# Kernel tuning notes

Measured on AMD Instinct MI355X. Metric: run time of the kernel, lower is better.

The kernel has to match this reference:

```python
import jax, jax.numpy as jnp
import numpy as np

N = 50000      # nodes
E = 800000     # edges
F_IN = 128     # input features
H = 64         # hidden channels
G = 64         # graphs in batch
EPS = 1e-5


def setup_inputs() -> dict:
    key = jax.random.key(0)
    ks = jax.random.split(key, 24)
    def nrm(k, s):
        return jax.random.normal(k, s, dtype=jnp.float32) * 0.05
    inp = {
        "x": nrm(ks[0], (N, F_IN)),
        "edge_index": jax.random.randint(ks[1], (2, E), 0, N),
        "batch": jnp.sort(jax.random.randint(ks[2], (N,), 0, G)),
        # GCNConv weights (stored [in, out]; math equivalent to torch Linear)
        "W0": nrm(ks[3], (F_IN, H)), "b0": nrm(ks[4], (H,)),
        "W1": nrm(ks[5], (H, H)),    "b1": nrm(ks[6], (H,)),
        "W2": nrm(ks[7], (H, H)),    "b2": nrm(ks[8], (H,)),
        # residual linears
        "RW0": nrm(ks[9], (F_IN, H)),  "rb0": nrm(ks[10], (H,)),
        "RW1": nrm(ks[11], (H, H)),    "rb1": nrm(ks[12], (H,)),
        "RW2": nrm(ks[13], (H, H)),    "rb2": nrm(ks[14], (H,)),
        # layernorm gamma/beta
        "g0": jnp.ones((H,), jnp.float32), "be0": jnp.zeros((H,), jnp.float32),
        "g1": jnp.ones((H,), jnp.float32), "be1": jnp.zeros((H,), jnp.float32),
        "g2": jnp.ones((H,), jnp.float32), "be2": jnp.zeros((H,), jnp.float32),
        # final readout linear
        "lw": nrm(ks[15], (H, 1)), "lb": nrm(ks[16], (1,)),
    }
    return inp


def _layernorm(x, g, b):
    mu = jnp.mean(x, axis=-1, keepdims=True)
    var = jnp.mean(jnp.square(x - mu), axis=-1, keepdims=True)
    return (x - mu) * jax.lax.rsqrt(var + EPS) * g + b


def reference(x, edge_index, batch,
              W0, b0, W1, b1, W2, b2,
              RW0, rb0, RW1, rb1, RW2, rb2,
              g0, be0, g1, be1, g2, be2,
              lw, lb):
    n = x.shape[0]
    loops = jnp.arange(n)
    row = jnp.concatenate([edge_index[0], loops])  # source
    col = jnp.concatenate([edge_index[1], loops])  # target
    # symmetric GCN normalization with self-loops (PyG gcn_norm)
    deg = jax.ops.segment_sum(jnp.ones_like(col, dtype=x.dtype), col, num_segments=n)
    dis = jnp.where(deg > 0, deg ** -0.5, 0.0)
    norm = dis[row] * dis[col]  # [E+N]

    params = [(W0, b0, RW0, rb0, g0, be0),
              (W1, b1, RW1, rb1, g1, be1),
              (W2, b2, RW2, rb2, g2, be2)]
    n_layers = len(params)
    for i, (W, b, RW, rb, g, be) in enumerate(params):
        h = x @ W                                                  # [n, H]
        agg = jax.ops.segment_sum(h[row] * norm[:, None], col, num_segments=n) + b
        x = agg + (x @ RW + rb)                                    # residual
        # dropout: eval mode -> identity
        x = _layernorm(x, g, be)
        if i < n_layers - 1:
            x = jax.nn.relu(x)

    # global mean pool over graphs
    counts = jax.ops.segment_sum(jnp.ones((n,), x.dtype), batch, num_segments=G)
    pooled = jax.ops.segment_sum(x, batch, num_segments=G) / jnp.maximum(counts, 1.0)[:, None]
    return pooled @ lw + lb  # [G, 1]
```

## Files before the change

kernel.cpp:

```cpp
#include <hip/hip_runtime.h>
#include <hip/hip_bf16.h>

#define HID 64
#define NGRAPH 64
#define BSH 7
#define NCH 384

static inline size_t align256(size_t x) { return (x + 255) & ~(size_t)255; }

typedef __attribute__((ext_vector_type(8))) short bf16x8;
typedef __attribute__((ext_vector_type(4))) float f32x4;

__device__ __forceinline__ float ldf(const void* p, size_t i, int f32) {
    if (f32) return ((const float*)p)[i];
    unsigned int w = ((unsigned int)((const unsigned short*)p)[i]) << 16;
    return __uint_as_float(w);
}
__device__ __forceinline__ float bf2f(unsigned short u) {
    return __uint_as_float(((unsigned int)u) << 16);
}
__device__ __forceinline__ unsigned short f2bf(float f) {
    __hip_bfloat16 h = __float2bfloat16(f);
    return *(unsigned short*)&h;
}

__device__ __forceinline__ unsigned char f2e4m3(float f) {
#if defined(__has_builtin) && __has_builtin(__builtin_amdgcn_cvt_pk_fp8_f32)
    int r = __builtin_amdgcn_cvt_pk_fp8_f32(f, f, 0, false);
    return (unsigned char)(r & 0xFF);
#else
    unsigned u = __float_as_uint(f);
    unsigned s = (u >> 24) & 0x80;
    unsigned a = u & 0x7FFFFFFF;
    float af = __uint_as_float(a);
    if (af < 0.015625f) {
        int m = (int)rintf(af * 512.f);
        return (unsigned char)(s | m);
    }
    unsigned r = a + 0x7FFFF + ((a >> 20) & 1);
    int e = (int)(r >> 23) - 127;
    if (e > 8) return (unsigned char)(s | 0x7E);
    return (unsigned char)(s | ((e + 7) << 3) | ((r >> 20) & 7));
#endif
}
template <int IDX>
__device__ __forceinline__ float d8(unsigned p) {
#if defined(__has_builtin) && __has_builtin(__builtin_amdgcn_cvt_f32_fp8)
    return __builtin_amdgcn_cvt_f32_fp8(p, IDX);
#else
    unsigned b = (p >> (IDX * 8)) & 0xFF;
    unsigned e = (b >> 3) & 0xF, m = b & 7;
    float v = e ? __uint_as_float(((e + 120) << 23) | (m << 20))
                : (float)m * (1.f / 512.f);
    return (b & 0x80) ? -v : v;
#endif
}

__global__ void k_sniff(const unsigned short* __restrict__ x, int nwords, int* __restrict__ flag,
                        float* __restrict__ gsum, int* __restrict__ gcnt) {
    __shared__ int cw, cz;
    int t = threadIdx.x;
    if (t == 0) { cw = 0; cz = 0; }
    if (t < NGRAPH) { gsum[t] = 0.f; gcnt[t] = 0; }
    __syncthreads();
    int weird = 0, evenzero = 0;
    for (int i = t; i < nwords; i += blockDim.x) {
        unsigned short u = x[i];
        int e = (u >> 7) & 0xFF;
        if (e >= 128) weird++;
        if (((i & 1) == 0) && ((u & 0x7FFF) == 0)) evenzero++;
    }
    atomicAdd(&cw, weird);
    atomicAdd(&cz, evenzero);
    __syncthreads();
    if (t == 0) *flag = (cw > nwords / 16 || cz > nwords / 8) ? 1 : 0;
}

__global__ __launch_bounds__(256) void k_prep(const int* __restrict__ batch, int* __restrict__ gcnt,
                                              int n, int nbG,
                                              const void* W0, const void* RW0, const void* b0, const void* rb0,
                                              const void* W1, const void* RW1, const void* b1, const void* rb1,
                                              const void* W2, const void* RW2, const void* b2, const void* rb2,
                                              const int* __restrict__ dflag,
                                              unsigned short* wt0, unsigned short* wt1, unsigned short* wt2,
                                              float* bcat,
                                              const int* __restrict__ ecol, int e, int nbuck,
                                              int* __restrict__ hist) {
    __shared__ int sh[1024];
    int b = blockIdx.x, t = threadIdx.x;
    if (b < nbG) {
        if (t < NGRAPH) sh[t] = 0;
        __syncthreads();
        int i = b * 256 + t;
        if (i < n) atomicAdd(&sh[batch[i]], 1);
        __syncthreads();
        if (t < NGRAPH && sh[t] > 0) atomicAdd(&gcnt[t], sh[t]);
    } else if (b < nbG + 130) {
        int f = *dflag;
        int i = (b - nbG) * 256 + t;
        if (i < 16384) {
            int nn = i >> 7, k = i & 127;
            float v = (nn < 64) ? ldf(W0, (size_t)k * 64 + nn, f) : ldf(RW0, (size_t)k * 64 + (nn - 64), f);
            wt0[nn * 128 + k] = f2bf(v);
        } else if (i < 24576) {
            int j = i - 16384; int nn = j >> 6, k = j & 63;
            float v = (nn < 64) ? ldf(W1, (size_t)k * 64 + nn, f) : ldf(RW1, (size_t)k * 64 + (nn - 64), f);
            wt1[nn * 64 + k] = f2bf(v);
        } else if (i < 32768) {
            int j = i - 24576; int nn = j >> 6, k = j & 63;
            float v = (nn < 64) ? ldf(W2, (size_t)k * 64 + nn, f) : ldf(RW2, (size_t)k * 64 + (nn - 64), f);
            wt2[nn * 64 + k] = f2bf(v);
        } else if (i < 32768 + 192) {
            int j = i - 32768; int l = j >> 6, c = j & 63;
            const void* bb = (l == 0) ? b0 : (l == 1) ? b1 : b2;
            const void* rr = (l == 0) ? rb0 : (l == 1) ? rb1 : rb2;
            bcat[l * 64 + c] = ldf(bb, c, f) + ldf(rr, c, f);
        }
    } else {
        int c = b - nbG - 130;
        for (int i = t; i < nbuck; i += 256) sh[i] = 0;
        __syncthreads();
        int per = (e + NCH - 1) / NCH;
        int s = c * per, en = min(e, s + per);
        for (int i = s + t; i < en; i += 256)
            atomicAdd(&sh[ecol[i] >> BSH], 1);
        __syncthreads();
        for (int i = t; i < nbuck; i += 256) hist[i * NCH + c] = sh[i];
    }
}

__global__ void k_scan1(const int* __restrict__ src, int* __restrict__ bsum, int n) {
    __shared__ int s[256];
    int t = threadIdx.x;
    int base = blockIdx.x * 1024 + t * 4;
    int sum = 0;
#pragma unroll
    for (int j = 0; j < 4; j++) { int i = base + j; if (i < n) sum += src[i]; }
    s[t] = sum;
    __syncthreads();
    for (int o = 128; o > 0; o >>= 1) {
        if (t < o) s[t] += s[t + o];
        __syncthreads();
    }
    if (t == 0) bsum[blockIdx.x] = s[0];
}

__global__ void k_scan2(const int* __restrict__ bsum, int* __restrict__ bscan,
                        int* __restrict__ out, int nb, int n) {
    __shared__ int s[256];
    int t = threadIdx.x;
    int v = (t < nb) ? bsum[t] : 0;
    s[t] = v;
    __syncthreads();
    for (int o = 1; o < 256; o <<= 1) {
        int x = (t >= o) ? s[t - o] : 0;
        __syncthreads();
        s[t] += x;
        __syncthreads();
    }
    if (t < nb) bscan[t] = s[t] - v;
    if (t == nb - 1) out[n] = s[t];
}

__global__ void k_scan3(const int* __restrict__ src, const int* __restrict__ bscan,
                        int* __restrict__ out, int n) {
    __shared__ int s[256];
    int t = threadIdx.x;
    int base = blockIdx.x * 1024 + t * 4;
    int tsum = 0;
#pragma unroll
    for (int j = 0; j < 4; j++) { int i = base + j; if (i < n) tsum += src[i]; }
    s[t] = tsum;
    __syncthreads();
    for (int o = 1; o < 256; o <<= 1) {
        int x = (t >= o) ? s[t - o] : 0;
        __syncthreads();
        s[t] += x;
        __syncthreads();
    }
    int off = bscan[blockIdx.x] + s[t] - tsum;
#pragma unroll
    for (int j = 0; j < 4; j++) {
        int i = base + j;
        if (i < n) { out[i] = off; off += src[i]; }
    }
}

__global__ __launch_bounds__(512) void k_scatter(const int* __restrict__ erow,
                                                 const int* __restrict__ ecol, int e, int nbuck,
                                                 const int* __restrict__ hoffs,
                                                 int* __restrict__ esrc,
                                                 unsigned char* __restrict__ et7) {
    __shared__ int cur[1024];
    int c = blockIdx.x, t = threadIdx.x;
    for (int i = t; i < nbuck; i += 512) cur[i] = hoffs[i * NCH + c];
    __syncthreads();
    int per = (e + NCH - 1) / NCH;
    int s = c * per, en = min(e, s + per);
    for (int i = s + t; i < en; i += 512) {
        int tg = ecol[i];
        int p = atomicAdd(&cur[tg >> BSH], 1);
        esrc[p] = erow[i];
        et7[p] = (unsigned char)(tg & 127);
    }
}

__global__ __launch_bounds__(256) void k_bucket(const int* __restrict__ esrc,
                                                const unsigned char* __restrict__ et7,
                                                const int* __restrict__ hoffs,
                                                int nbuck, int n, int e,
                                                int* __restrict__ offs, float* __restrict__ dis,
                                                int* __restrict__ csr) {
    __shared__ int hist[128];
    __shared__ int lofs[128];
    __shared__ int curs[128];
    int b = blockIdx.x, t = threadIdx.x;
    int nb0 = b << BSH;
    int nn = n - nb0; if (nn > 128) nn = 128;
    int s = hoffs[b * NCH];
    int en = (b + 1 < nbuck) ? hoffs[(b + 1) * NCH] : e;
    if (t < 128) hist[t] = 0;
    __syncthreads();
    for (int i = s + t; i < en; i += 256)
        atomicAdd(&hist[et7[i]], 1);
    __syncthreads();
    if (t < 128) lofs[t] = hist[t];
    __syncthreads();
    for (int o = 1; o < 128; o <<= 1) {
        int v = (t < 128 && t >= o) ? lofs[t - o] : 0;
        __syncthreads();
        if (t < 128) lofs[t] += v;
        __syncthreads();
    }
    if (t < nn) {
        int ex = s + lofs[t] - hist[t];
        offs[nb0 + t] = ex;
        curs[t] = ex;
        dis[nb0 + t] = rsqrtf((float)(hist[t] + 1));
    }
    if (b == nbuck - 1 && t == 0) offs[n] = e;
    __syncthreads();
    for (int i = s + t; i < en; i += 256) {
        int p = atomicAdd(&curs[et7[i]], 1);
        csr[p] = esrc[i];
    }
}

template <int K, bool XFLAG, bool LO>
__global__ __launch_bounds__(256) void k_gemm(const void* __restrict__ xin,
                                              const unsigned short* __restrict__ wt,
                                              const float* __restrict__ bcat,
                                              const float* __restrict__ dis,
                                              const int* __restrict__ dflag,
                                              unsigned char* __restrict__ hs,
                                              float* __restrict__ base, int n) {
    const int KP = K + 8;
    __shared__ unsigned short sXh[64 * KP];
    __shared__ unsigned short sXl[LO ? 64 * KP : 1];
    int f32 = *dflag;
    int tid = threadIdx.x;
    int row0 = blockIdx.x * 64;

    if (XFLAG && !f32) {
        const uint4* xv = (const uint4*)xin;
        const int C = K / 8;
        for (int i = tid; i < 64 * C; i += 256) {
            int r = i / C, c = i % C;
            int gr = row0 + r;
            uint4 v = (gr < n) ? xv[(size_t)gr * C + c] : make_uint4(0, 0, 0, 0);
            *(uint4*)&sXh[r * KP + c * 8] = v;
        }
    } else if (XFLAG) {
        for (int i = tid; i < 64 * K; i += 256) {
            int r = i / K, k = i - r * K;
            int gr = row0 + r;
            float v = (gr < n) ? ((const float*)xin)[(size_t)gr * K + k] : 0.f;
            sXh[r * KP + k] = f2bf(v);
        }
    } else {
        const float4* xv = (const float4*)xin;
        const int C = K / 4;
        for (int i = tid; i < 64 * C; i += 256) {
            int r = i / C, c = i % C;
            int gr = row0 + r;
            float4 v = (gr < n) ? xv[(size_t)gr * C + c] : make_float4(0.f, 0.f, 0.f, 0.f);
            ushort4 h, lo;
            h.x = f2bf(v.x); h.y = f2bf(v.y); h.z = f2bf(v.z); h.w = f2bf(v.w);
            if (LO) {
                lo.x = f2bf(v.x - bf2f(h.x)); lo.y = f2bf(v.y - bf2f(h.y));
                lo.z = f2bf(v.z - bf2f(h.z)); lo.w = f2bf(v.w - bf2f(h.w));
            }
            *(ushort4*)&sXh[r * KP + c * 4] = h;
            if (LO) *(ushort4*)&sXl[r * KP + c * 4] = lo;
        }
    }
    __syncthreads();

    int w = tid >> 6, lane = tid & 63;
    int m = lane & 15, q = lane >> 4;
    f32x4 acc[8];
#pragma unroll
    for (int ct = 0; ct < 8; ct++) acc[ct] = (f32x4){0.f, 0.f, 0.f, 0.f};

    int arow = w * 16 + m;
#pragma unroll
    for (int ks = 0; ks < K / 32; ks++) {
        int ka = ks * 32 + q * 8;
        bf16x8 ah = *(const bf16x8*)&sXh[arow * KP + ka];
        bf16x8 al;
        if (LO) al = *(const bf16x8*)&sXl[arow * KP + ka];
#pragma unroll
        for (int ct = 0; ct < 8; ct++) {
            bf16x8 bb = *(const bf16x8*)(wt + (size_t)(ct * 16 + m) * K + ka);
            acc[ct] = __builtin_amdgcn_mfma_f32_16x16x32_bf16(ah, bb, acc[ct], 0, 0, 0);
            if (LO) acc[ct] = __builtin_amdgcn_mfma_f32_16x16x32_bf16(al, bb, acc[ct], 0, 0, 0);
        }
    }

#pragma unroll
    for (int ct = 0; ct < 4; ct++) {
        int col = ct * 16 + m;
#pragma unroll
        for (int reg = 0; reg < 4; reg++) {
            int r = row0 + w * 16 + q * 4 + reg;
            if (r < n) {
                float dv = dis[r];
                float h = acc[ct][reg] * dv;
                hs[(size_t)r * 64 + col] = f2e4m3(h);
                base[(size_t)r * 64 + col] = h * dv + acc[ct + 4][reg] + bcat[col];
            }
        }
    }
}

template <bool FINAL>
__global__ __launch_bounds__(1024) void k_agg_ln(const unsigned char* __restrict__ hs,
                                                 const float* __restrict__ base,
                                                 const float* __restrict__ dis,
                                                 const int* __restrict__ offs,
                                                 const int* __restrict__ csr,
                                                 const void* __restrict__ gam,
                                                 const void* __restrict__ bet,
                                                 const int* __restrict__ dflag,
                                                 float* __restrict__ xout, int n, int relu,
                                                 const int* __restrict__ batch,
                                                 const void* __restrict__ lw,
                                                 float* __restrict__ gsum) {
    __shared__ float sG[FINAL ? NGRAPH : 1];
    int f32 = *dflag;
    int t = threadIdx.x;
    if (FINAL) {
        if (t < NGRAPH) sG[t] = 0.f;
        __syncthreads();
    }
    int grp = t >> 4;
    int l = t & 15;
    int gl0 = (t & 63) & ~15;
    int v = blockIdx.x * 64 + grp;
    if (v < n) {
        int s = offs[v];
        int e2 = offs[v + 1];
        float4 bv = *(const float4*)&base[(size_t)v * 64 + l * 4];
        float dv = dis[v];
        float a0 = 0.f, a1 = 0.f, a2 = 0.f, a3 = 0.f;
        for (int gbase = s; gbase < e2; gbase += 16) {
            int cnt = e2 - gbase; if (cnt > 16) cnt = 16;
            int cur = (gbase + l < e2) ? csr[gbase + l] : 0;
            if (cnt == 16) {
                unsigned pp[16];
#pragma unroll
                for (int j = 0; j < 16; j++) {
                    int sj = __shfl(cur, gl0 + j, 64);
                    pp[j] = *(const unsigned*)(hs + (size_t)sj * 64 + l * 4);
                }
#pragma unroll
                for (int j = 0; j < 16; j++) {
                    a0 += d8<0>(pp[j]);
                    a1 += d8<1>(pp[j]);
                    a2 += d8<2>(pp[j]);
                    a3 += d8<3>(pp[j]);
                }
            } else {
                int j = 0;
                for (; j + 7 < cnt; j += 8) {
                    unsigned pp[8];
#pragma unroll
                    for (int u = 0; u < 8; u++) {
                        int sj = __shfl(cur, gl0 + j + u, 64);
                        pp[u] = *(const unsigned*)(hs + (size_t)sj * 64 + l * 4);
                    }
#pragma unroll
                    for (int u = 0; u < 8; u++) {
                        a0 += d8<0>(pp[u]);
                        a1 += d8<1>(pp[u]);
                        a2 += d8<2>(pp[u]);
                        a3 += d8<3>(pp[u]);
                    }
                }
                for (; j + 3 < cnt; j += 4) {
                    unsigned pp[4];
#pragma unroll
                    for (int u = 0; u < 4; u++) {
                        int sj = __shfl(cur, gl0 + j + u, 64);
                        pp[u] = *(const unsigned*)(hs + (size_t)sj * 64 + l * 4);
                    }
#pragma unroll
                    for (int u = 0; u < 4; u++) {
                        a0 += d8<0>(pp[u]);
                        a1 += d8<1>(pp[u]);
                        a2 += d8<2>(pp[u]);
                        a3 += d8<3>(pp[u]);
                    }
                }
                for (; j < cnt; j++) {
                    int sj = __shfl(cur, gl0 + j, 64);
                    unsigned p0 = *(const unsigned*)(hs + (size_t)sj * 64 + l * 4);
                    a0 += d8<0>(p0);
                    a1 += d8<1>(p0);
                    a2 += d8<2>(p0);
                    a3 += d8<3>(p0);
                }
            }
        }
        a0 = bv.x + dv * a0;
        a1 = bv.y + dv * a1;
        a2 = bv.z + dv * a2;
        a3 = bv.w + dv * a3;
        float m = a0 + a1 + a2 + a3;
        m += __shfl_xor(m, 1, 64); m += __shfl_xor(m, 2, 64);
        m += __shfl_xor(m, 4, 64); m += __shfl_xor(m, 8, 64);
        m *= (1.f / 64.f);
        float d0 = a0 - m, d1 = a1 - m, d2 = a2 - m, d3 = a3 - m;
        float var = d0 * d0 + d1 * d1 + d2 * d2 + d3 * d3;
        var += __shfl_xor(var, 1, 64); var += __shfl_xor(var, 2, 64);
        var += __shfl_xor(var, 4, 64); var += __shfl_xor(var, 8, 64);
        var *= (1.f / 64.f);
        float rs = rsqrtf(var + 1e-5f);
        float y0 = d0 * rs * ldf(gam, l * 4 + 0, f32) + ldf(bet, l * 4 + 0, f32);
        float y1 = d1 * rs * ldf(gam, l * 4 + 1, f32) + ldf(bet, l * 4 + 1, f32);
        float y2 = d2 * rs * ldf(gam, l * 4 + 2, f32) + ldf(bet, l * 4 + 2, f32);
        float y3 = d3 * rs * ldf(gam, l * 4 + 3, f32) + ldf(bet, l * 4 + 3, f32);
        if (relu) {
            y0 = fmaxf(y0, 0.f); y1 = fmaxf(y1, 0.f);
            y2 = fmaxf(y2, 0.f); y3 = fmaxf(y3, 0.f);
        }
        if (!FINAL) {
            *(float4*)&xout[(size_t)v * 64 + l * 4] = make_float4(y0, y1, y2, y3);
        } else {
            float val = y0 * ldf(lw, l * 4 + 0, f32) + y1 * ldf(lw, l * 4 + 1, f32)
                      + y2 * ldf(lw, l * 4 + 2, f32) + y3 * ldf(lw, l * 4 + 3, f32);
            val += __shfl_xor(val, 1, 64); val += __shfl_xor(val, 2, 64);
            val += __shfl_xor(val, 4, 64); val += __shfl_xor(val, 8, 64);
            if (l == 0) atomicAdd(&sG[batch[v]], val);
        }
    }
    if (FINAL) {
        __syncthreads();
        if (t < NGRAPH && sG[t] != 0.f) atomicAdd(&gsum[t], sG[t]);
    }
}

__global__ void k_final(const float* __restrict__ gsum, const int* __restrict__ gcnt,
                        const void* __restrict__ lb, const int* __restrict__ dflag,
                        void* __restrict__ out, int g) {
    int f32 = *dflag;
    int i = threadIdx.x;
    if (i < g) {
        float c = fmaxf((float)gcnt[i], 1.f);
        float v = gsum[i] / c + ldf(lb, 0, f32);
        if (f32) ((float*)out)[i] = v;
        else ((__hip_bfloat16*)out)[i] = __float2bfloat16(v);
    }
}

extern "C" void kernel_launch(void* const* d_in, const int* in_sizes, int n_in,
                              void* d_out, int out_size, void* d_ws, size_t ws_size,
                              hipStream_t stream) {
    const void* x_in = d_in[0];
    const int* edge_index = (const int*)d_in[1];
    const int* batch = (const int*)d_in[2];
    const void *W0 = d_in[3], *b0 = d_in[4], *W1 = d_in[5], *b1 = d_in[6],
               *W2 = d_in[7], *b2 = d_in[8];
    const void *RW0 = d_in[9], *rb0 = d_in[10], *RW1 = d_in[11], *rb1 = d_in[12],
               *RW2 = d_in[13], *rb2 = d_in[14];
    const void *g0 = d_in[15], *be0 = d_in[16], *g1 = d_in[17], *be1 = d_in[18],
               *g2 = d_in[19], *be2 = d_in[20], *lw = d_in[21], *lb = d_in[22];

    const int N = in_sizes[2];
    const int E = in_sizes[1] / 2;
    const int* erow = edge_index;
    const int* ecol = edge_index + E;
    const int nbuck = (N + 127) >> BSH;
    const int T = nbuck * NCH;

    char* p = (char*)d_ws;
    size_t off = 0;
    float* dis = (float*)(p + off);  off = align256(off + (size_t)N * 4);
    int* offs = (int*)(p + off);     off = align256(off + (size_t)(N + 1) * 4);
    int* csr = (int*)(p + off);      off = align256(off + (size_t)E * 4);
    int* esrc = (int*)(p + off);     off = align256(off + (size_t)E * 4);
    unsigned char* et7 = (unsigned char*)(p + off); off = align256(off + (size_t)E);
    int* hist = (int*)(p + off);     off = align256(off + (size_t)T * 4);
    int* hoffs = (int*)(p + off);    off = align256(off + (size_t)(T + 1) * 4);
    unsigned char* hs = (unsigned char*)(p + off); off = align256(off + (size_t)N * HID);
    float* base = (float*)(p + off); off = align256(off + (size_t)N * HID * 4);
    float* xbuf = (float*)(p + off); off = align256(off + (size_t)N * HID * 4);
    unsigned short* wt0 = (unsigned short*)(p + off); off = align256(off + 16384 * 2);
    unsigned short* wt1 = (unsigned short*)(p + off); off = align256(off + 8192 * 2);
    unsigned short* wt2 = (unsigned short*)(p + off); off = align256(off + 8192 * 2);
    float* bcat = (float*)(p + off); off = align256(off + 192 * 4);
    int* bsum = (int*)(p + off);     off = align256(off + 256 * 4);
    int* bscan = (int*)(p + off);    off = align256(off + 256 * 4);
    float* gsum = (float*)(p + off); off = align256(off + NGRAPH * 4);
    int* gcnt = (int*)(p + off);     off = align256(off + NGRAPH * 4);
    int* dflag = (int*)(p + off);    off = align256(off + 4);
    (void)ws_size;

    const int TB = 256;
    int nbG = (N + TB - 1) / TB;
    int nbT = (T + 1023) / 1024;
    int nb_gemm = (N + 63) / 64;
    int nb_agg = (N + 63) / 64;

    k_sniff<<<1, 256, 0, stream>>>((const unsigned short*)x_in, 8192, dflag, gsum, gcnt);
    k_prep<<<nbG + 130 + NCH, TB, 0, stream>>>(batch, gcnt, N, nbG,
                                               W0, RW0, b0, rb0, W1, RW1, b1, rb1,
                                               W2, RW2, b2, rb2, dflag, wt0, wt1, wt2, bcat,
                                               ecol, E, nbuck, hist);
    k_scan1<<<nbT, TB, 0, stream>>>(hist, bsum, T);
    k_scan2<<<1, TB, 0, stream>>>(bsum, bscan, hoffs, nbT, T);
    k_scan3<<<nbT, TB, 0, stream>>>(hist, bscan, hoffs, T);
    k_scatter<<<NCH, 512, 0, stream>>>(erow, ecol, E, nbuck, hoffs, esrc, et7);
    k_bucket<<<nbuck, TB, 0, stream>>>(esrc, et7, hoffs, nbuck, N, E, offs, dis, csr);

    k_gemm<128, true, false><<<nb_gemm, TB, 0, stream>>>(x_in, wt0, bcat, dis, dflag, hs, base, N);
    k_agg_ln<false><<<nb_agg, 1024, 0, stream>>>(hs, base, dis, offs, csr, g0, be0, dflag,
                                                 xbuf, N, 1, nullptr, nullptr, nullptr);
    k_gemm<64, false, true><<<nb_gemm, TB, 0, stream>>>(xbuf, wt1, bcat + 64, dis, dflag, hs, base, N);
    k_agg_ln<false><<<nb_agg, 1024, 0, stream>>>(hs, base, dis, offs, csr, g1, be1, dflag,
                                                 xbuf, N, 1, nullptr, nullptr, nullptr);
    k_gemm<64, false, true><<<nb_gemm, TB, 0, stream>>>(xbuf, wt2, bcat + 128, dis, dflag, hs, base, N);
    k_agg_ln<true><<<nb_agg, 1024, 0, stream>>>(hs, base, dis, offs, csr, g2, be2, dflag,
                                                nullptr, N, 0, batch, lw, gsum);

    k_final<<<1, 64, 0, stream>>>(gsum, gcnt, lb, dflag, d_out, NGRAPH);
}
```

Before: 305.8 us.

## Fuse next-layer GEMM into aggregation-layernorm kernel and stage weights in LDS

The aggregation plus layernorm kernel now also runs the next layer's GEMM on its 64-row tile. It splits the normalized output into bf16 hi/lo parts in shared memory and runs MFMA against weights staged in LDS. This drops the fp32 xbuf round trip through global memory and two GEMM launches, using ping-pong hs/base buffers instead. The standalone layer-0 GEMM also stages its weights in LDS, and the scatter kernel drops from 512 to 256 threads per block. The costs are more LDS use and a barrier in the 1024-thread kernel, which may lower occupancy.

```diff
diff --git a/kernel.cpp b/kernel.cpp
--- a/kernel.cpp
+++ b/kernel.cpp
@@ -186,18 +186,18 @@
     }
 }
 
-__global__ __launch_bounds__(512) void k_scatter(const int* __restrict__ erow,
+__global__ __launch_bounds__(256) void k_scatter(const int* __restrict__ erow,
                                                  const int* __restrict__ ecol, int e, int nbuck,
                                                  const int* __restrict__ hoffs,
                                                  int* __restrict__ esrc,
                                                  unsigned char* __restrict__ et7) {
     __shared__ int cur[1024];
     int c = blockIdx.x, t = threadIdx.x;
-    for (int i = t; i < nbuck; i += 512) cur[i] = hoffs[i * NCH + c];
+    for (int i = t; i < nbuck; i += 256) cur[i] = hoffs[i * NCH + c];
     __syncthreads();
     int per = (e + NCH - 1) / NCH;
     int s = c * per, en = min(e, s + per);
-    for (int i = s + t; i < en; i += 512) {
+    for (int i = s + t; i < en; i += 256) {
         int tg = ecol[i];
         int p = atomicAdd(&cur[tg >> BSH], 1);
         esrc[p] = erow[i];
@@ -257,10 +257,21 @@
     const int KP = K + 8;
     __shared__ unsigned short sXh[64 * KP];
     __shared__ unsigned short sXl[LO ? 64 * KP : 1];
+    __shared__ unsigned short sW[128 * KP];
     int f32 = *dflag;
     int tid = threadIdx.x;
     int row0 = blockIdx.x * 64;
 
+    {
+        const uint4* src = (const uint4*)wt;
+        uint4* dst = (uint4*)sW;
+        const int C = K / 8;
+        const int CP = KP / 8;
+        for (int i = tid; i < 128 * C; i += 256) {
+            int nrow = i / C, c = i % C;
+            dst[nrow * CP + c] = src[i];
+        }
+    }
     if (XFLAG && !f32) {
         const uint4* xv = (const uint4*)xin;
         const int C = K / 8;
@@ -311,7 +322,7 @@
         if (LO) al = *(const bf16x8*)&sXl[arow * KP + ka];
 #pragma unroll
         for (int ct = 0; ct < 8; ct++) {
-            bf16x8 bb = *(const bf16x8*)(wt + (size_t)(ct * 16 + m) * K + ka);
+            bf16x8 bb = *(const bf16x8*)&sW[(ct * 16 + m) * KP + ka];
             acc[ct] = __builtin_amdgcn_mfma_f32_16x16x32_bf16(ah, bb, acc[ct], 0, 0, 0);
             if (LO) acc[ct] = __builtin_amdgcn_mfma_f32_16x16x32_bf16(al, bb, acc[ct], 0, 0, 0);
         }
@@ -333,93 +344,92 @@
     }
 }
 
-template <bool FINAL>
-__global__ __launch_bounds__(1024) void k_agg_ln(const unsigned char* __restrict__ hs,
-                                                 const float* __restrict__ base,
-                                                 const float* __restrict__ dis,
-                                                 const int* __restrict__ offs,
-                                                 const int* __restrict__ csr,
-                                                 const void* __restrict__ gam,
-                                                 const void* __restrict__ bet,
-                                                 const int* __restrict__ dflag,
-                                                 float* __restrict__ xout, int n, int relu,
-                                                 const int* __restrict__ batch,
-                                                 const void* __restrict__ lw,
-                                                 float* __restrict__ gsum) {
-    __shared__ float sG[FINAL ? NGRAPH : 1];
+template <bool GN>
+__global__ __launch_bounds__(1024) void k_fagg(const unsigned char* __restrict__ hs_in,
+                                               const float* __restrict__ base_in,
+                                               const float* __restrict__ dis,
+                                               const int* __restrict__ offs,
+                                               const int* __restrict__ csr,
+                                               const void* __restrict__ gam,
+                                               const void* __restrict__ bet,
+                                               const int* __restrict__ dflag,
+                                               int n, int relu,
+                                               const unsigned short* __restrict__ wt,
+                                               const float* __restrict__ bcat,
+                                               unsigned char* __restrict__ hs_out,
+                                               float* __restrict__ base_out,
+                                               const int* __restrict__ batch,
+                                               const void* __restrict__ lw,
+                                               float* __restrict__ gsum) {
+    __shared__ unsigned short sYh[GN ? 64 * 72 : 1];
+    __shared__ unsigned short sYl[GN ? 64 * 72 : 1];
+    __shared__ unsigned short sW[GN ? 128 * 72 : 1];
+    __shared__ float sG[GN ? 1 : NGRAPH];
+    int t = threadIdx.x;
     int f32 = *dflag;
-    int t = threadIdx.x;
-    if (FINAL) {
+    if (GN) {
+        const uint4* src = (const uint4*)wt;
+        uint4* dst = (uint4*)sW;
+        int nrow = t >> 3, c = t & 7;
+        dst[nrow * 9 + c] = src[t];
+    } else {
         if (t < NGRAPH) sG[t] = 0.f;
         __syncthreads();
     }
+
     int grp = t >> 4;
     int l = t & 15;
     int gl0 = (t & 63) & ~15;
-    int v = blockIdx.x * 64 + grp;
+    int row0 = blockIdx.x * 64;
+    int v = row0 + grp;
+    float y0 = 0.f, y1 = 0.f, y2 = 0.f, y3 = 0.f;
     if (v < n) {
         int s = offs[v];
         int e2 = offs[v + 1];
-        float4 bv = *(const float4*)&base[(size_t)v * 64 + l * 4];
+        float4 bv = *(const float4*)&base_in[(size_t)v * 64 + l * 4];
         float dv = dis[v];
         float a0 = 0.f, a1 = 0.f, a2 = 0.f, a3 = 0.f;
         for (int gbase = s; gbase < e2; gbase += 16) {
             int cnt = e2 - gbase; if (cnt > 16) cnt = 16;
             int cur = (gbase + l < e2) ? csr[gbase + l] : 0;
-            if (cnt == 16) {
-                unsigned pp[16];
-#pragma unroll
-                for (int j = 0; j < 16; j++) {
-                    int sj = __shfl(cur, gl0 + j, 64);
-                    pp[j] = *(const unsigned*)(hs + (size_t)sj * 64 + l * 4);
+            int j = 0;
+            for (; j + 7 < cnt; j += 8) {
+                unsigned pp[8];
+#pragma unroll
+                for (int u = 0; u < 8; u++) {
+                    int sj = __shfl(cur, gl0 + j + u, 64);
+                    pp[u] = *(const unsigned*)(hs_in + (size_t)sj * 64 + l * 4);
                 }
 #pragma unroll
-                for (int j = 0; j < 16; j++) {
-                    a0 += d8<0>(pp[j]);
-                    a1 += d8<1>(pp[j]);
-                    a2 += d8<2>(pp[j]);
-                    a3 += d8<3>(pp[j]);
+                for (int u = 0; u < 8; u++) {
+                    a0 += d8<0>(pp[u]);
+                    a1 += d8<1>(pp[u]);
+                    a2 += d8<2>(pp[u]);
+                    a3 += d8<3>(pp[u]);
                 }
-            } else {
-                int j = 0;
-                for (; j + 7 < cnt; j += 8) {
-                    unsigned pp[8];
-#pragma unroll
-                    for (int u = 0; u < 8; u++) {
-                        int sj = __shfl(cur, gl0 + j + u, 64);
-                        pp[u] = *(const unsigned*)(hs + (size_t)sj * 64 + l * 4);
-                    }
-#pragma unroll
-                    for (int u = 0; u < 8; u++) {
-                        a0 += d8<0>(pp[u]);
-                        a1 += d8<1>(pp[u]);
-                        a2 += d8<2>(pp[u]);
-                        a3 += d8<3>(pp[u]);
-                    }
+            }
+            for (; j + 3 < cnt; j += 4) {
+                unsigned pp[4];
+#pragma unroll
+                for (int u = 0; u < 4; u++) {
+                    int sj = __shfl(cur, gl0 + j + u, 64);
+                    pp[u] = *(const unsigned*)(hs_in + (size_t)sj * 64 + l * 4);
                 }
-                for (; j + 3 < cnt; j += 4) {
-                    unsigned pp[4];
-#pragma unroll
-                    for (int u = 0; u < 4; u++) {
-                        int sj = __shfl(cur, gl0 + j + u, 64);
-                        pp[u] = *(const unsigned*)(hs + (size_t)sj * 64 + l * 4);
-                    }
-#pragma unroll
-                    for (int u = 0; u < 4; u++) {
-                        a0 += d8<0>(pp[u]);
-                        a1 += d8<1>(pp[u]);
-                        a2 += d8<2>(pp[u]);
-                        a3 += d8<3>(pp[u]);
-                    }
+#pragma unroll
+                for (int u = 0; u < 4; u++) {
+                    a0 += d8<0>(pp[u]);
+                    a1 += d8<1>(pp[u]);
+                    a2 += d8<2>(pp[u]);
+                    a3 += d8<3>(pp[u]);
                 }
-                for (; j < cnt; j++) {
-                    int sj = __shfl(cur, gl0 + j, 64);
-                    unsigned p0 = *(const unsigned*)(hs + (size_t)sj * 64 + l * 4);
-                    a0 += d8<0>(p0);
-                    a1 += d8<1>(p0);
-                    a2 += d8<2>(p0);
-                    a3 += d8<3>(p0);
-                }
+            }
+            for (; j < cnt; j++) {
+                int sj = __shfl(cur, gl0 + j, 64);
+                unsigned p0 = *(const unsigned*)(hs_in + (size_t)sj * 64 + l * 4);
+                a0 += d8<0>(p0);
+                a1 += d8<1>(p0);
+                a2 += d8<2>(p0);
+                a3 += d8<3>(p0);
             }
         }
         a0 = bv.x + dv * a0;
@@ -436,27 +446,68 @@
         var += __shfl_xor(var, 4, 64); var += __shfl_xor(var, 8, 64);
         var *= (1.f / 64.f);
         float rs = rsqrtf(var + 1e-5f);
-        float y0 = d0 * rs * ldf(gam, l * 4 + 0, f32) + ldf(bet, l * 4 + 0, f32);
-        float y1 = d1 * rs * ldf(gam, l * 4 + 1, f32) + ldf(bet, l * 4 + 1, f32);
-        float y2 = d2 * rs * ldf(gam, l * 4 + 2, f32) + ldf(bet, l * 4 + 2, f32);
-        float y3 = d3 * rs * ldf(gam, l * 4 + 3, f32) + ldf(bet, l * 4 + 3, f32);
+        y0 = d0 * rs * ldf(gam, l * 4 + 0, f32) + ldf(bet, l * 4 + 0, f32);
+        y1 = d1 * rs * ldf(gam, l * 4 + 1, f32) + ldf(bet, l * 4 + 1, f32);
+        y2 = d2 * rs * ldf(gam, l * 4 + 2, f32) + ldf(bet, l * 4 + 2, f32);
+        y3 = d3 * rs * ldf(gam, l * 4 + 3, f32) + ldf(bet, l * 4 + 3, f32);
         if (relu) {
             y0 = fmaxf(y0, 0.f); y1 = fmaxf(y1, 0.f);
             y2 = fmaxf(y2, 0.f); y3 = fmaxf(y3, 0.f);
         }
-        if (!FINAL) {
-            *(float4*)&xout[(size_t)v * 64 + l * 4] = make_float4(y0, y1, y2, y3);
-        } else {
+    }
+
+    if (!GN) {
+        if (v < n) {
             float val = y0 * ldf(lw, l * 4 + 0, f32) + y1 * ldf(lw, l * 4 + 1, f32)
                       + y2 * ldf(lw, l * 4 + 2, f32) + y3 * ldf(lw, l * 4 + 3, f32);
             val += __shfl_xor(val, 1, 64); val += __shfl_xor(val, 2, 64);
             val += __shfl_xor(val, 4, 64); val += __shfl_xor(val, 8, 64);
             if (l == 0) atomicAdd(&sG[batch[v]], val);
         }
-    }
-    if (FINAL) {
         __syncthreads();
         if (t < NGRAPH && sG[t] != 0.f) atomicAdd(&gsum[t], sG[t]);
+        return;
+    }
+
+    {
+        ushort4 h, lo;
+        h.x = f2bf(y0); h.y = f2bf(y1); h.z = f2bf(y2); h.w = f2bf(y3);
+        lo.x = f2bf(y0 - bf2f(h.x)); lo.y = f2bf(y1 - bf2f(h.y));
+        lo.z = f2bf(y2 - bf2f(h.z)); lo.w = f2bf(y3 - bf2f(h.w));
+        if (v >= n) { h = make_ushort4(0, 0, 0, 0); lo = make_ushort4(0, 0, 0, 0); }
+        *(ushort4*)&sYh[grp * 72 + l * 4] = h;
+        *(ushort4*)&sYl[grp * 72 + l * 4] = lo;
+    }
+    __syncthreads();
+
+    int ww = t >> 6, lane = t & 63;
+    int m = lane & 15, q = lane >> 4;
+    int rt = ww & 3, c2 = ww >> 2;
+    f32x4 accW = (f32x4){0.f, 0.f, 0.f, 0.f};
+    f32x4 accR = (f32x4){0.f, 0.f, 0.f, 0.f};
+    int arow = rt * 16 + m;
+#pragma unroll
+    for (int ks = 0; ks < 2; ks++) {
+        int ka = ks * 32 + q * 8;
+        bf16x8 ah = *(const bf16x8*)&sYh[arow * 72 + ka];
+        bf16x8 al = *(const bf16x8*)&sYl[arow * 72 + ka];
+        bf16x8 bW = *(const bf16x8*)&sW[(c2 * 16 + m) * 72 + ka];
+        bf16x8 bR = *(const bf16x8*)&sW[((c2 + 4) * 16 + m) * 72 + ka];
+        accW = __builtin_amdgcn_mfma_f32_16x16x32_bf16(ah, bW, accW, 0, 0, 0);
+        accW = __builtin_amdgcn_mfma_f32_16x16x32_bf16(al, bW, accW, 0, 0, 0);
+        accR = __builtin_amdgcn_mfma_f32_16x16x32_bf16(ah, bR, accR, 0, 0, 0);
+        accR = __builtin_amdgcn_mfma_f32_16x16x32_bf16(al, bR, accR, 0, 0, 0);
+    }
+    int col = c2 * 16 + m;
+#pragma unroll
+    for (int reg = 0; reg < 4; reg++) {
+        int r = row0 + rt * 16 + q * 4 + reg;
+        if (r < n) {
+            float dv = dis[r];
+            float h = accW[reg] * dv;
+            hs_out[(size_t)r * 64 + col] = f2e4m3(h);
+            base_out[(size_t)r * 64 + col] = h * dv + accR[reg] + bcat[col];
+        }
     }
 }
 
@@ -502,9 +553,10 @@
     unsigned char* et7 = (unsigned char*)(p + off); off = align256(off + (size_t)E);
     int* hist = (int*)(p + off);     off = align256(off + (size_t)T * 4);
     int* hoffs = (int*)(p + off);    off = align256(off + (size_t)(T + 1) * 4);
-    unsigned char* hs = (unsigned char*)(p + off); off = align256(off + (size_t)N * HID);
-    float* base = (float*)(p + off); off = align256(off + (size_t)N * HID * 4);
-    float* xbuf = (float*)(p + off); off = align256(off + (size_t)N * HID * 4);
+    unsigned char* hsA = (unsigned char*)(p + off); off = align256(off + (size_t)N * HID);
+    unsigned char* hsB = (unsigned char*)(p + off); off = align256(off + (size_t)N * HID);
+    float* baseA = (float*)(p + off); off = align256(off + (size_t)N * HID * 4);
+    float* baseB = (float*)(p + off); off = align256(off + (size_t)N * HID * 4);
     unsigned short* wt0 = (unsigned short*)(p + off); off = align256(off + 16384 * 2);
     unsigned short* wt1 = (unsigned short*)(p + off); off = align256(off + 8192 * 2);
     unsigned short* wt2 = (unsigned short*)(p + off); off = align256(off + 8192 * 2);
@@ -530,18 +582,16 @@
     k_scan1<<<nbT, TB, 0, stream>>>(hist, bsum, T);
     k_scan2<<<1, TB, 0, stream>>>(bsum, bscan, hoffs, nbT, T);
     k_scan3<<<nbT, TB, 0, stream>>>(hist, bscan, hoffs, T);
-    k_scatter<<<NCH, 512, 0, stream>>>(erow, ecol, E, nbuck, hoffs, esrc, et7);
+    k_scatter<<<NCH, TB, 0, stream>>>(erow, ecol, E, nbuck, hoffs, esrc, et7);
     k_bucket<<<nbuck, TB, 0, stream>>>(esrc, et7, hoffs, nbuck, N, E, offs, dis, csr);
 
-    k_gemm<128, true, false><<<nb_gemm, TB, 0, stream>>>(x_in, wt0, bcat, dis, dflag, hs, base, N);
-    k_agg_ln<false><<<nb_agg, 1024, 0, stream>>>(hs, base, dis, offs, csr, g0, be0, dflag,
-                                                 xbuf, N, 1, nullptr, nullptr, nullptr);
-    k_gemm<64, false, true><<<nb_gemm, TB, 0, stream>>>(xbuf, wt1, bcat + 64, dis, dflag, hs, base, N);
-    k_agg_ln<false><<<nb_agg, 1024, 0, stream>>>(hs, base, dis, offs, csr, g1, be1, dflag,
-                                                 xbuf, N, 1, nullptr, nullptr, nullptr);
-    k_gemm<64, false, true><<<nb_gemm, TB, 0, stream>>>(xbuf, wt2, bcat + 128, dis, dflag, hs, base, N);
-    k_agg_ln<true><<<nb_agg, 1024, 0, stream>>>(hs, base, dis, offs, csr, g2, be2, dflag,
-                                                nullptr, N, 0, batch, lw, gsum);
+    k_gemm<128, true, false><<<nb_gemm, TB, 0, stream>>>(x_in, wt0, bcat, dis, dflag, hsA, baseA, N);
+    k_fagg<true><<<nb_agg, 1024, 0, stream>>>(hsA, baseA, dis, offs, csr, g0, be0, dflag, N, 1,
+                                              wt1, bcat + 64, hsB, baseB, nullptr, nullptr, nullptr);
+    k_fagg<true><<<nb_agg, 1024, 0, stream>>>(hsB, baseB, dis, offs, csr, g1, be1, dflag, N, 1,
+                                              wt2, bcat + 128, hsA, baseA, nullptr, nullptr, nullptr);
+    k_fagg<false><<<nb_agg, 1024, 0, stream>>>(hsA, baseA, dis, offs, csr, g2, be2, dflag, N, 0,
+                                               nullptr, nullptr, nullptr, nullptr, batch, lw, gsum);
 
     k_final<<<1, 64, 0, stream>>>(gsum, gcnt, lb, dflag, d_out, NGRAPH);
 }
```

Measured after the change: 267.6 us. 12.5% less time.
